# Kernel tuning notes

Measured on AMD Instinct MI355X. Metric: run time of the kernel, lower is better.

## Reference

```python
import jax, jax.numpy as jnp
import numpy as np

B, T, F, H = 2048, 512, 32, 128  # batch, seq_len, input_features, hidden_units

def _xavier(key, shape):
    fan_in, fan_out = shape[1], shape[0]
    limit = float(np.sqrt(6.0 / (fan_in + fan_out)))
    return jax.random.uniform(key, shape, jnp.float32, -limit, limit)

def setup_inputs() -> dict:
    key = jax.random.key(0)
    ks = jax.random.split(key, 8)
    x = jax.random.normal(ks[0], (B, T, F), jnp.float32)
    # PyTorch LSTM weights: weight_ih_l{k} [4H, in], weight_hh_l{k} [4H, H]; biases init to zeros.
    Wih0 = _xavier(ks[1], (4 * H, F))
    Whh0 = _xavier(ks[2], (4 * H, H))
    b0 = jnp.zeros((4 * H,), jnp.float32)  # b_ih + b_hh (both zero-init)
    Wih1 = _xavier(ks[3], (4 * H, H))
    Whh1 = _xavier(ks[4], (4 * H, H))
    b1 = jnp.zeros((4 * H,), jnp.float32)
    Wfc = _xavier(ks[5], (1, H))
    bfc = jnp.zeros((1,), jnp.float32)
    return dict(x=x, Wih0=Wih0, Whh0=Whh0, b0=b0, Wih1=Wih1, Whh1=Whh1, b1=b1, Wfc=Wfc, bfc=bfc)

def _lstm_layer(x, Wih, Whh, b):
    # x: [B, T, Din] -> outputs h over time: [B, T, H]
    pre = jnp.einsum('btf,gf->btg', x, Wih) + b  # precompute input projections [B, T, 4H]
    h0 = jnp.zeros((x.shape[0], Whh.shape[1]), x.dtype)

    def step(carry, p_t):
        h, c = carry
        z = p_t + h @ Whh.T  # [B, 4H]
        i, f, g, o = jnp.split(z, 4, axis=-1)  # PyTorch gate order: i, f, g, o
        i = jax.nn.sigmoid(i)
        f = jax.nn.sigmoid(f)
        g = jnp.tanh(g)
        o = jax.nn.sigmoid(o)
        c = f * c + i * g
        h = o * jnp.tanh(c)
        return (h, c), h

    (_, _), hs = jax.lax.scan(step, (h0, h0), jnp.swapaxes(pre, 0, 1))  # hs: [T, B, H]
    return jnp.swapaxes(hs, 0, 1)

def reference(x, Wih0, Whh0, b0, Wih1, Whh1, b1, Wfc, bfc):
    h = _lstm_layer(x, Wih0, Whh0, b0)   # layer 0 (dropout off in eval)
    h = _lstm_layer(h, Wih1, Whh1, b1)   # layer 1
    last = h[:, -1, :]                   # [B, H]
    return last @ Wfc.T + bfc            # [B, 1]
```

## Files before the change

### kernel.cpp

```cpp
#include <hip/hip_runtime.h>
#include <stdint.h>


#define B_ 2048
#define T_ 512
#define F_ 32
#define H_ 128
#define LSTR 144
#define H0SZ (8 * LSTR)
#define WIH1_NSTR 520
#define WIH1_WSTR (16 * WIH1_NSTR)

#define LOG2E 1.4426950408889634f

typedef _Float16 half8 __attribute__((ext_vector_type(8)));
typedef float float4_t __attribute__((ext_vector_type(4)));

#define BARRIER_LGKM() asm volatile("s_waitcnt lgkmcnt(0)\n\ts_barrier" ::: "memory")

__device__ __forceinline__ float fexp2(float x) {
  float r; asm("v_exp_f32 %0, %1" : "=v"(r) : "v"(x)); return r;
}
__device__ __forceinline__ float frcp(float x) { return __builtin_amdgcn_rcpf(x); }

__device__ __forceinline__ half8 cvt2f4(float4_t a, float4_t b) {
  half8 r;
  r[0] = (_Float16)a[0]; r[1] = (_Float16)a[1]; r[2] = (_Float16)a[2]; r[3] = (_Float16)a[3];
  r[4] = (_Float16)b[0]; r[5] = (_Float16)b[1]; r[6] = (_Float16)b[2]; r[7] = (_Float16)b[3];
  return r;
}
__device__ __forceinline__ half8 load8cvt(const float* p) {
  return cvt2f4(*(const float4_t*)p, *(const float4_t*)(p + 4));
}

__global__ __launch_bounds__(512, 2) void lstm_fused(
    const float* __restrict__ x, const float* __restrict__ Wih0,
    const float* __restrict__ Whh0, const float* __restrict__ b0,
    const float* __restrict__ Wih1, const float* __restrict__ Whh1,
    const float* __restrict__ b1, const float* __restrict__ Wfc,
    const float* __restrict__ bfc, float* __restrict__ out)
{
  __shared__ __attribute__((aligned(16))) _Float16 lds_wih1[8 * WIH1_WSTR];
  __shared__ __attribute__((aligned(16))) _Float16 lds_h0[2 * H0SZ];
  __shared__ __attribute__((aligned(16))) _Float16 lds_h1[2 * H0SZ];
  __shared__ float lds_fc[8][8];

  const int tid  = threadIdx.x;
  const int w    = tid >> 6;
  const int lane = tid & 63;
  const int n    = lane & 15;
  const int q    = lane >> 4;
  const int rbase = (int)blockIdx.x * 8;
  const int rload = rbase + (n & 7);
  const int rsh  = (q >> 1) * 2;
  const int rowq = (q & 1) * 4;
  const int colg = w * 16 + n;
  const int aoff = (n & 7) * LSTR + q * 8;

  half8 bwih0[4], bwhh0[4][4], bwhh1[4][4];
  _Float16* wslot = lds_wih1 + w * WIH1_WSTR + n * WIH1_NSTR + q * 8;
#pragma unroll
  for (int j = 0; j < 4; ++j) {
    const int g = j * H_ + colg;
    bwih0[j] = load8cvt(Wih0 + g * F_ + q * 8);
#pragma unroll
    for (int kc = 0; kc < 4; ++kc) {
      bwhh0[j][kc] = load8cvt(Whh0 + g * H_ + kc * 32 + q * 8);
      bwhh1[j][kc] = load8cvt(Whh1 + g * H_ + kc * 32 + q * 8);
      *(half8*)(wslot + (j * 4 + kc) * 32) = load8cvt(Wih1 + g * H_ + kc * 32 + q * 8);
    }
  }
  const float cI0 = -b0[0 * H_ + colg] * LOG2E;
  const float cF0 = -b0[1 * H_ + colg] * LOG2E;
  const float cG0 =  b0[2 * H_ + colg] * (2.0f * LOG2E);
  const float cO0 = -b0[3 * H_ + colg] * LOG2E;
  const float cI1 = -b1[0 * H_ + colg] * LOG2E;
  const float cF1 = -b1[1 * H_ + colg] * LOG2E;
  const float cG1 =  b1[2 * H_ + colg] * (2.0f * LOG2E);
  const float cO1 = -b1[3 * H_ + colg] * LOG2E;
  const float wfc = Wfc[colg];

  for (int i = tid; i < 2 * H0SZ; i += 512) { lds_h0[i] = (_Float16)0.0f; lds_h1[i] = (_Float16)0.0f; }
  __syncthreads();

  const float4_t zC = {0.f, 0.f, 0.f, 0.f};
  float c00 = 0.f, c01 = 0.f;
  float c10 = 0.f, c11 = 0.f;
  float hl0 = 0.f, hl1 = 0.f;

  const float* xptr = x + rload * (T_ * F_) + q * 8;
  float4_t xrA = *(const float4_t*)(xptr);
  float4_t xrB = *(const float4_t*)(xptr + 4);

#pragma unroll 1
  for (int tau = 0; tau <= T_; ++tau) {
    const int pw = tau & 1;
    _Float16* h0rd = lds_h0 + (pw ^ 1) * H0SZ;
    _Float16* h0wr = lds_h0 + pw * H0SZ;
    _Float16* h1rd = lds_h1 + pw * H0SZ;
    _Float16* h1wr = lds_h1 + (pw ^ 1) * H0SZ;
    const bool do0 = (tau < T_), do1 = (tau >= 1);

    half8 ah[4];
#pragma unroll
    for (int kc = 0; kc < 4; ++kc)
      ah[kc] = *(const half8*)(h0rd + aoff + kc * 32);

    float4_t acc0[4], acc1[4];
    if (do0) {
      half8 ax = cvt2f4(xrA, xrB);
#pragma unroll
      for (int j = 0; j < 4; ++j)
        acc0[j] = __builtin_amdgcn_mfma_f32_16x16x32_f16(ax, bwih0[j], zC, 0, 0, 0);
#pragma unroll
      for (int kc = 0; kc < 4; ++kc)
#pragma unroll
        for (int j = 0; j < 4; ++j)
          acc0[j] = __builtin_amdgcn_mfma_f32_16x16x32_f16(ah[kc], bwhh0[j][kc], acc0[j], 0, 0, 0);
      const int tn = (tau + 1 < T_) ? tau + 1 : T_ - 1;
      xrA = *(const float4_t*)(xptr + tn * F_);
      xrB = *(const float4_t*)(xptr + tn * F_ + 4);
    }
    if (do1) {
      half8 a1h[4];
#pragma unroll
      for (int kc = 0; kc < 4; ++kc)
        a1h[kc] = *(const half8*)(h1rd + aoff + kc * 32);
#pragma unroll
      for (int kc = 0; kc < 4; ++kc) {
        half8 f0 = *(const half8*)(wslot + (0 * 4 + kc) * 32);
        half8 f1 = *(const half8*)(wslot + (1 * 4 + kc) * 32);
        half8 f2 = *(const half8*)(wslot + (2 * 4 + kc) * 32);
        half8 f3 = *(const half8*)(wslot + (3 * 4 + kc) * 32);
        acc1[0] = __builtin_amdgcn_mfma_f32_16x16x32_f16(ah[kc], f0, kc == 0 ? zC : acc1[0], 0, 0, 0);
        acc1[1] = __builtin_amdgcn_mfma_f32_16x16x32_f16(ah[kc], f1, kc == 0 ? zC : acc1[1], 0, 0, 0);
        acc1[2] = __builtin_amdgcn_mfma_f32_16x16x32_f16(ah[kc], f2, kc == 0 ? zC : acc1[2], 0, 0, 0);
        acc1[3] = __builtin_amdgcn_mfma_f32_16x16x32_f16(ah[kc], f3, kc == 0 ? zC : acc1[3], 0, 0, 0);
      }
#pragma unroll
      for (int kc = 0; kc < 4; ++kc)
#pragma unroll
        for (int j = 0; j < 4; ++j)
          acc1[j] = __builtin_amdgcn_mfma_f32_16x16x32_f16(a1h[kc], bwhh1[j][kc], acc1[j], 0, 0, 0);
    }

    if (do0) {
#pragma unroll
      for (int rr = 0; rr < 2; ++rr) {
        const int ri = rsh + rr;
        const float gi = frcp(1.0f + fexp2(__builtin_fmaf(acc0[0][ri], -LOG2E, cI0)));
        const float gf = frcp(1.0f + fexp2(__builtin_fmaf(acc0[1][ri], -LOG2E, cF0)));
        const float gg = 1.0f - 2.0f * frcp(1.0f + fexp2(__builtin_fmaf(acc0[2][ri], 2.0f * LOG2E, cG0)));
        const float go = frcp(1.0f + fexp2(__builtin_fmaf(acc0[3][ri], -LOG2E, cO0)));
        float& cc = rr ? c01 : c00;
        cc = __builtin_fmaf(gf, cc, gi * gg);
        const float th = 1.0f - 2.0f * frcp(1.0f + fexp2(cc * (2.0f * LOG2E)));
        h0wr[(rowq + ri) * LSTR + colg] = (_Float16)(go * th);
      }
    }
    if (do1) {
#pragma unroll
      for (int rr = 0; rr < 2; ++rr) {
        const int ri = rsh + rr;
        const float gi = frcp(1.0f + fexp2(__builtin_fmaf(acc1[0][ri], -LOG2E, cI1)));
        const float gf = frcp(1.0f + fexp2(__builtin_fmaf(acc1[1][ri], -LOG2E, cF1)));
        const float gg = 1.0f - 2.0f * frcp(1.0f + fexp2(__builtin_fmaf(acc1[2][ri], 2.0f * LOG2E, cG1)));
        const float go = frcp(1.0f + fexp2(__builtin_fmaf(acc1[3][ri], -LOG2E, cO1)));
        float& cc = rr ? c11 : c10;
        cc = __builtin_fmaf(gf, cc, gi * gg);
        const float th = 1.0f - 2.0f * frcp(1.0f + fexp2(cc * (2.0f * LOG2E)));
        const float hv = go * th;
        h1wr[(rowq + ri) * LSTR + colg] = (_Float16)hv;
        if (rr) hl1 = hv; else hl0 = hv;
      }
    }
    BARRIER_LGKM();
  }

  float p0 = hl0 * wfc, p1 = hl1 * wfc;
#pragma unroll
  for (int m = 1; m < 16; m <<= 1) {
    p0 += __shfl_xor(p0, m);
    p1 += __shfl_xor(p1, m);
  }
  if (n == 0) {
    lds_fc[w][rowq + rsh + 0] = p0;
    lds_fc[w][rowq + rsh + 1] = p1;
  }
  __syncthreads();
  if (tid < 8) {
    float s = bfc[0];
#pragma unroll
    for (int wv = 0; wv < 8; ++wv) s += lds_fc[wv][tid];
    out[rbase + tid] = s;
  }
}

extern "C" void kernel_launch(void* const* d_in, const int* in_sizes, int n_in,
                              void* d_out, int out_size, void* d_ws, size_t ws_size,
                              hipStream_t stream) {
  const float* x    = (const float*)d_in[0];
  const float* Wih0 = (const float*)d_in[1];
  const float* Whh0 = (const float*)d_in[2];
  const float* b0   = (const float*)d_in[3];
  const float* Wih1 = (const float*)d_in[4];
  const float* Whh1 = (const float*)d_in[5];
  const float* b1   = (const float*)d_in[6];
  const float* Wfc  = (const float*)d_in[7];
  const float* bfc  = (const float*)d_in[8];
  float* outp = (float*)d_out;
  (void)d_ws; (void)ws_size;

  lstm_fused<<<B_ / 8, 512, 0, stream>>>(x, Wih0, Whh0, b0, Wih1, Whh1, b1,
                                         Wfc, bfc, outp);
}
```

Before: 1.054 ms.

## Hold half of Wih1 in registers, reorder layer-1 MFMAs, pack biases to fp16

Half of the layer-1 input weights (first two K-chunks) now stay in registers, and the remaining half moves to a smaller, contiguous LDS layout that is loaded in two staged groups interleaved with the MFMA chain. Layer-1 MFMAs move after the layer-0 gate math, so layer-0 h is written before layer-1 work. Biases are packed into one fp16 vector and the final h1 is read back from LDS, both to cut live registers. The goal is to reduce LDS traffic and latency per step while staying within the 2-blocks-per-CU register budget. The risks are spilling from extra register weights and lost precision in the fp16 biases and fp16 final h.

```diff
diff --git a/kernel.cpp b/kernel.cpp
--- a/kernel.cpp
+++ b/kernel.cpp
@@ -8,8 +8,7 @@
 #define H_ 128
 #define LSTR 144
 #define H0SZ (8 * LSTR)
-#define WIH1_NSTR 520
-#define WIH1_WSTR (16 * WIH1_NSTR)
+#define W1STR 4096
 
 #define LOG2E 1.4426950408889634f
 
@@ -40,7 +39,7 @@
     const float* __restrict__ b1, const float* __restrict__ Wfc,
     const float* __restrict__ bfc, float* __restrict__ out)
 {
-  __shared__ __attribute__((aligned(16))) _Float16 lds_wih1[8 * WIH1_WSTR];
+  __shared__ __attribute__((aligned(16))) _Float16 lds_w1[8 * W1STR];
   __shared__ __attribute__((aligned(16))) _Float16 lds_h0[2 * H0SZ];
   __shared__ __attribute__((aligned(16))) _Float16 lds_h1[2 * H0SZ];
   __shared__ float lds_fc[8][8];
@@ -57,8 +56,8 @@
   const int colg = w * 16 + n;
   const int aoff = (n & 7) * LSTR + q * 8;
 
-  half8 bwih0[4], bwhh0[4][4], bwhh1[4][4];
-  _Float16* wslot = lds_wih1 + w * WIH1_WSTR + n * WIH1_NSTR + q * 8;
+  half8 bwih0[4], bwhh0[4][4], bwhh1[4][4], bwih1r[2][4];
+  _Float16* w1base = lds_w1 + w * W1STR + q * 128 + n * 8;
 #pragma unroll
   for (int j = 0; j < 4; ++j) {
     const int g = j * H_ + colg;
@@ -67,18 +66,21 @@
     for (int kc = 0; kc < 4; ++kc) {
       bwhh0[j][kc] = load8cvt(Whh0 + g * H_ + kc * 32 + q * 8);
       bwhh1[j][kc] = load8cvt(Whh1 + g * H_ + kc * 32 + q * 8);
-      *(half8*)(wslot + (j * 4 + kc) * 32) = load8cvt(Wih1 + g * H_ + kc * 32 + q * 8);
-    }
-  }
-  const float cI0 = -b0[0 * H_ + colg] * LOG2E;
-  const float cF0 = -b0[1 * H_ + colg] * LOG2E;
-  const float cG0 =  b0[2 * H_ + colg] * (2.0f * LOG2E);
-  const float cO0 = -b0[3 * H_ + colg] * LOG2E;
-  const float cI1 = -b1[0 * H_ + colg] * LOG2E;
-  const float cF1 = -b1[1 * H_ + colg] * LOG2E;
-  const float cG1 =  b1[2 * H_ + colg] * (2.0f * LOG2E);
-  const float cO1 = -b1[3 * H_ + colg] * LOG2E;
-  const float wfc = Wfc[colg];
+    }
+    bwih1r[0][j] = load8cvt(Wih1 + g * H_ + 0 * 32 + q * 8);
+    bwih1r[1][j] = load8cvt(Wih1 + g * H_ + 1 * 32 + q * 8);
+    *(half8*)(w1base + (j * 2 + 0) * 512) = load8cvt(Wih1 + g * H_ + 2 * 32 + q * 8);
+    *(half8*)(w1base + (j * 2 + 1) * 512) = load8cvt(Wih1 + g * H_ + 3 * 32 + q * 8);
+  }
+  half8 cpack;
+  cpack[0] = (_Float16)(-b0[0 * H_ + colg] * LOG2E);
+  cpack[1] = (_Float16)(-b0[1 * H_ + colg] * LOG2E);
+  cpack[2] = (_Float16)( b0[2 * H_ + colg] * (2.0f * LOG2E));
+  cpack[3] = (_Float16)(-b0[3 * H_ + colg] * LOG2E);
+  cpack[4] = (_Float16)(-b1[0 * H_ + colg] * LOG2E);
+  cpack[5] = (_Float16)(-b1[1 * H_ + colg] * LOG2E);
+  cpack[6] = (_Float16)( b1[2 * H_ + colg] * (2.0f * LOG2E));
+  cpack[7] = (_Float16)(-b1[3 * H_ + colg] * LOG2E);
 
   for (int i = tid; i < 2 * H0SZ; i += 512) { lds_h0[i] = (_Float16)0.0f; lds_h1[i] = (_Float16)0.0f; }
   __syncthreads();
@@ -86,7 +88,6 @@
   const float4_t zC = {0.f, 0.f, 0.f, 0.f};
   float c00 = 0.f, c01 = 0.f;
   float c10 = 0.f, c11 = 0.f;
-  float hl0 = 0.f, hl1 = 0.f;
 
   const float* xptr = x + rload * (T_ * F_) + q * 8;
   float4_t xrA = *(const float4_t*)(xptr);
@@ -105,8 +106,12 @@
 #pragma unroll
     for (int kc = 0; kc < 4; ++kc)
       ah[kc] = *(const half8*)(h0rd + aoff + kc * 32);
-
-    float4_t acc0[4], acc1[4];
+    half8 w1s0[4];
+#pragma unroll
+    for (int j = 0; j < 4; ++j)
+      w1s0[j] = *(const half8*)(w1base + (j * 2 + 0) * 512);
+
+    float4_t acc0[4];
     if (do0) {
       half8 ax = cvt2f4(xrA, xrB);
 #pragma unroll
@@ -121,37 +126,14 @@
       xrA = *(const float4_t*)(xptr + tn * F_);
       xrB = *(const float4_t*)(xptr + tn * F_ + 4);
     }
-    if (do1) {
-      half8 a1h[4];
-#pragma unroll
-      for (int kc = 0; kc < 4; ++kc)
-        a1h[kc] = *(const half8*)(h1rd + aoff + kc * 32);
-#pragma unroll
-      for (int kc = 0; kc < 4; ++kc) {
-        half8 f0 = *(const half8*)(wslot + (0 * 4 + kc) * 32);
-        half8 f1 = *(const half8*)(wslot + (1 * 4 + kc) * 32);
-        half8 f2 = *(const half8*)(wslot + (2 * 4 + kc) * 32);
-        half8 f3 = *(const half8*)(wslot + (3 * 4 + kc) * 32);
-        acc1[0] = __builtin_amdgcn_mfma_f32_16x16x32_f16(ah[kc], f0, kc == 0 ? zC : acc1[0], 0, 0, 0);
-        acc1[1] = __builtin_amdgcn_mfma_f32_16x16x32_f16(ah[kc], f1, kc == 0 ? zC : acc1[1], 0, 0, 0);
-        acc1[2] = __builtin_amdgcn_mfma_f32_16x16x32_f16(ah[kc], f2, kc == 0 ? zC : acc1[2], 0, 0, 0);
-        acc1[3] = __builtin_amdgcn_mfma_f32_16x16x32_f16(ah[kc], f3, kc == 0 ? zC : acc1[3], 0, 0, 0);
-      }
-#pragma unroll
-      for (int kc = 0; kc < 4; ++kc)
-#pragma unroll
-        for (int j = 0; j < 4; ++j)
-          acc1[j] = __builtin_amdgcn_mfma_f32_16x16x32_f16(a1h[kc], bwhh1[j][kc], acc1[j], 0, 0, 0);
-    }
-
     if (do0) {
 #pragma unroll
       for (int rr = 0; rr < 2; ++rr) {
         const int ri = rsh + rr;
-        const float gi = frcp(1.0f + fexp2(__builtin_fmaf(acc0[0][ri], -LOG2E, cI0)));
-        const float gf = frcp(1.0f + fexp2(__builtin_fmaf(acc0[1][ri], -LOG2E, cF0)));
-        const float gg = 1.0f - 2.0f * frcp(1.0f + fexp2(__builtin_fmaf(acc0[2][ri], 2.0f * LOG2E, cG0)));
-        const float go = frcp(1.0f + fexp2(__builtin_fmaf(acc0[3][ri], -LOG2E, cO0)));
+        const float gi = frcp(1.0f + fexp2(__builtin_fmaf(acc0[0][ri], -LOG2E, (float)cpack[0])));
+        const float gf = frcp(1.0f + fexp2(__builtin_fmaf(acc0[1][ri], -LOG2E, (float)cpack[1])));
+        const float gg = 1.0f - 2.0f * frcp(1.0f + fexp2(__builtin_fmaf(acc0[2][ri], 2.0f * LOG2E, (float)cpack[2])));
+        const float go = frcp(1.0f + fexp2(__builtin_fmaf(acc0[3][ri], -LOG2E, (float)cpack[3])));
         float& cc = rr ? c01 : c00;
         cc = __builtin_fmaf(gf, cc, gi * gg);
         const float th = 1.0f - 2.0f * frcp(1.0f + fexp2(cc * (2.0f * LOG2E)));
@@ -159,25 +141,51 @@
       }
     }
     if (do1) {
+      float4_t acc1[4];
+#pragma unroll
+      for (int j = 0; j < 4; ++j)
+        acc1[j] = __builtin_amdgcn_mfma_f32_16x16x32_f16(ah[0], bwih1r[0][j], zC, 0, 0, 0);
+#pragma unroll
+      for (int j = 0; j < 4; ++j)
+        acc1[j] = __builtin_amdgcn_mfma_f32_16x16x32_f16(ah[1], bwih1r[1][j], acc1[j], 0, 0, 0);
+#pragma unroll
+      for (int j = 0; j < 4; ++j)
+        acc1[j] = __builtin_amdgcn_mfma_f32_16x16x32_f16(ah[2], w1s0[j], acc1[j], 0, 0, 0);
+      half8 w1s1[4];
+#pragma unroll
+      for (int j = 0; j < 4; ++j)
+        w1s1[j] = *(const half8*)(w1base + (j * 2 + 1) * 512);
+      half8 a1h[4];
+#pragma unroll
+      for (int kc = 0; kc < 4; ++kc)
+        a1h[kc] = *(const half8*)(h1rd + aoff + kc * 32);
+#pragma unroll
+      for (int j = 0; j < 4; ++j)
+        acc1[j] = __builtin_amdgcn_mfma_f32_16x16x32_f16(ah[3], w1s1[j], acc1[j], 0, 0, 0);
+#pragma unroll
+      for (int kc = 0; kc < 4; ++kc)
+#pragma unroll
+        for (int j = 0; j < 4; ++j)
+          acc1[j] = __builtin_amdgcn_mfma_f32_16x16x32_f16(a1h[kc], bwhh1[j][kc], acc1[j], 0, 0, 0);
 #pragma unroll
       for (int rr = 0; rr < 2; ++rr) {
         const int ri = rsh + rr;
-        const float gi = frcp(1.0f + fexp2(__builtin_fmaf(acc1[0][ri], -LOG2E, cI1)));
-        const float gf = frcp(1.0f + fexp2(__builtin_fmaf(acc1[1][ri], -LOG2E, cF1)));
-        const float gg = 1.0f - 2.0f * frcp(1.0f + fexp2(__builtin_fmaf(acc1[2][ri], 2.0f * LOG2E, cG1)));
-        const float go = frcp(1.0f + fexp2(__builtin_fmaf(acc1[3][ri], -LOG2E, cO1)));
+        const float gi = frcp(1.0f + fexp2(__builtin_fmaf(acc1[0][ri], -LOG2E, (float)cpack[4])));
+        const float gf = frcp(1.0f + fexp2(__builtin_fmaf(acc1[1][ri], -LOG2E, (float)cpack[5])));
+        const float gg = 1.0f - 2.0f * frcp(1.0f + fexp2(__builtin_fmaf(acc1[2][ri], 2.0f * LOG2E, (float)cpack[6])));
+        const float go = frcp(1.0f + fexp2(__builtin_fmaf(acc1[3][ri], -LOG2E, (float)cpack[7])));
         float& cc = rr ? c11 : c10;
         cc = __builtin_fmaf(gf, cc, gi * gg);
         const float th = 1.0f - 2.0f * frcp(1.0f + fexp2(cc * (2.0f * LOG2E)));
-        const float hv = go * th;
-        h1wr[(rowq + ri) * LSTR + colg] = (_Float16)hv;
-        if (rr) hl1 = hv; else hl0 = hv;
+        h1wr[(rowq + ri) * LSTR + colg] = (_Float16)(go * th);
       }
     }
     BARRIER_LGKM();
   }
 
-  float p0 = hl0 * wfc, p1 = hl1 * wfc;
+  const float wfcv = Wfc[colg];
+  float p0 = (float)lds_h1[H0SZ + (rowq + rsh + 0) * LSTR + colg] * wfcv;
+  float p1 = (float)lds_h1[H0SZ + (rowq + rsh + 1) * LSTR + colg] * wfcv;
 #pragma unroll
   for (int m = 1; m < 16; m <<= 1) {
     p0 += __shfl_xor(p0, m);
```

After: 1.234 ms. +17.0%, slower.

## Reorder layer-1 MFMA schedule with double-buffered Wih1 LDS fragments and conflict-free layout

Applied to the files above, without the earlier changes.

The LDS layout of the layer-1 input weights changes to a lane-contiguous stride (q*128 + n*8) that avoids bank conflicts. Loads of those fragments are spread across the loop, double-buffered between w1a and w1b, and the layer-1 MFMAs move after the layer-0 gate math so the LDS reads overlap with compute. The final FC reads h1 from LDS in fp16 instead of keeping fp32 copies in registers, which saves registers but adds a little rounding error.

```diff
diff --git a/kernel.cpp b/kernel.cpp
--- a/kernel.cpp
+++ b/kernel.cpp
@@ -8,8 +8,7 @@
 #define H_ 128
 #define LSTR 144
 #define H0SZ (8 * LSTR)
-#define WIH1_NSTR 520
-#define WIH1_WSTR (16 * WIH1_NSTR)
+#define W1STR 8192
 
 #define LOG2E 1.4426950408889634f
 
@@ -40,7 +39,7 @@
     const float* __restrict__ b1, const float* __restrict__ Wfc,
     const float* __restrict__ bfc, float* __restrict__ out)
 {
-  __shared__ __attribute__((aligned(16))) _Float16 lds_wih1[8 * WIH1_WSTR];
+  __shared__ __attribute__((aligned(16))) _Float16 lds_w1[8 * W1STR];
   __shared__ __attribute__((aligned(16))) _Float16 lds_h0[2 * H0SZ];
   __shared__ __attribute__((aligned(16))) _Float16 lds_h1[2 * H0SZ];
   __shared__ float lds_fc[8][8];
@@ -58,7 +57,7 @@
   const int aoff = (n & 7) * LSTR + q * 8;
 
   half8 bwih0[4], bwhh0[4][4], bwhh1[4][4];
-  _Float16* wslot = lds_wih1 + w * WIH1_WSTR + n * WIH1_NSTR + q * 8;
+  _Float16* w1base = lds_w1 + w * W1STR + q * 128 + n * 8;
 #pragma unroll
   for (int j = 0; j < 4; ++j) {
     const int g = j * H_ + colg;
@@ -67,7 +66,7 @@
     for (int kc = 0; kc < 4; ++kc) {
       bwhh0[j][kc] = load8cvt(Whh0 + g * H_ + kc * 32 + q * 8);
       bwhh1[j][kc] = load8cvt(Whh1 + g * H_ + kc * 32 + q * 8);
-      *(half8*)(wslot + (j * 4 + kc) * 32) = load8cvt(Wih1 + g * H_ + kc * 32 + q * 8);
+      *(half8*)(w1base + (kc * 4 + j) * 512) = load8cvt(Wih1 + g * H_ + kc * 32 + q * 8);
     }
   }
   const float cI0 = -b0[0 * H_ + colg] * LOG2E;
@@ -78,7 +77,6 @@
   const float cF1 = -b1[1 * H_ + colg] * LOG2E;
   const float cG1 =  b1[2 * H_ + colg] * (2.0f * LOG2E);
   const float cO1 = -b1[3 * H_ + colg] * LOG2E;
-  const float wfc = Wfc[colg];
 
   for (int i = tid; i < 2 * H0SZ; i += 512) { lds_h0[i] = (_Float16)0.0f; lds_h1[i] = (_Float16)0.0f; }
   __syncthreads();
@@ -86,7 +84,6 @@
   const float4_t zC = {0.f, 0.f, 0.f, 0.f};
   float c00 = 0.f, c01 = 0.f;
   float c10 = 0.f, c11 = 0.f;
-  float hl0 = 0.f, hl1 = 0.f;
 
   const float* xptr = x + rload * (T_ * F_) + q * 8;
   float4_t xrA = *(const float4_t*)(xptr);
@@ -105,8 +102,12 @@
 #pragma unroll
     for (int kc = 0; kc < 4; ++kc)
       ah[kc] = *(const half8*)(h0rd + aoff + kc * 32);
-
-    float4_t acc0[4], acc1[4];
+    half8 w1a[4];
+#pragma unroll
+    for (int j = 0; j < 4; ++j)
+      w1a[j] = *(const half8*)(w1base + (0 * 4 + j) * 512);
+
+    float4_t acc0[4];
     if (do0) {
       half8 ax = cvt2f4(xrA, xrB);
 #pragma unroll
@@ -121,29 +122,6 @@
       xrA = *(const float4_t*)(xptr + tn * F_);
       xrB = *(const float4_t*)(xptr + tn * F_ + 4);
     }
-    if (do1) {
-      half8 a1h[4];
-#pragma unroll
-      for (int kc = 0; kc < 4; ++kc)
-        a1h[kc] = *(const half8*)(h1rd + aoff + kc * 32);
-#pragma unroll
-      for (int kc = 0; kc < 4; ++kc) {
-        half8 f0 = *(const half8*)(wslot + (0 * 4 + kc) * 32);
-        half8 f1 = *(const half8*)(wslot + (1 * 4 + kc) * 32);
-        half8 f2 = *(const half8*)(wslot + (2 * 4 + kc) * 32);
-        half8 f3 = *(const half8*)(wslot + (3 * 4 + kc) * 32);
-        acc1[0] = __builtin_amdgcn_mfma_f32_16x16x32_f16(ah[kc], f0, kc == 0 ? zC : acc1[0], 0, 0, 0);
-        acc1[1] = __builtin_amdgcn_mfma_f32_16x16x32_f16(ah[kc], f1, kc == 0 ? zC : acc1[1], 0, 0, 0);
-        acc1[2] = __builtin_amdgcn_mfma_f32_16x16x32_f16(ah[kc], f2, kc == 0 ? zC : acc1[2], 0, 0, 0);
-        acc1[3] = __builtin_amdgcn_mfma_f32_16x16x32_f16(ah[kc], f3, kc == 0 ? zC : acc1[3], 0, 0, 0);
-      }
-#pragma unroll
-      for (int kc = 0; kc < 4; ++kc)
-#pragma unroll
-        for (int j = 0; j < 4; ++j)
-          acc1[j] = __builtin_amdgcn_mfma_f32_16x16x32_f16(a1h[kc], bwhh1[j][kc], acc1[j], 0, 0, 0);
-    }
-
     if (do0) {
 #pragma unroll
       for (int rr = 0; rr < 2; ++rr) {
@@ -159,6 +137,38 @@
       }
     }
     if (do1) {
+      float4_t acc1[4];
+      half8 w1b[4];
+#pragma unroll
+      for (int j = 0; j < 4; ++j)
+        w1b[j] = *(const half8*)(w1base + (1 * 4 + j) * 512);
+#pragma unroll
+      for (int j = 0; j < 4; ++j)
+        acc1[j] = __builtin_amdgcn_mfma_f32_16x16x32_f16(ah[0], w1a[j], zC, 0, 0, 0);
+#pragma unroll
+      for (int j = 0; j < 4; ++j)
+        w1a[j] = *(const half8*)(w1base + (2 * 4 + j) * 512);
+#pragma unroll
+      for (int j = 0; j < 4; ++j)
+        acc1[j] = __builtin_amdgcn_mfma_f32_16x16x32_f16(ah[1], w1b[j], acc1[j], 0, 0, 0);
+#pragma unroll
+      for (int j = 0; j < 4; ++j)
+        w1b[j] = *(const half8*)(w1base + (3 * 4 + j) * 512);
+#pragma unroll
+      for (int j = 0; j < 4; ++j)
+        acc1[j] = __builtin_amdgcn_mfma_f32_16x16x32_f16(ah[2], w1a[j], acc1[j], 0, 0, 0);
+      half8 a1h[4];
+#pragma unroll
+      for (int kc = 0; kc < 4; ++kc)
+        a1h[kc] = *(const half8*)(h1rd + aoff + kc * 32);
+#pragma unroll
+      for (int j = 0; j < 4; ++j)
+        acc1[j] = __builtin_amdgcn_mfma_f32_16x16x32_f16(ah[3], w1b[j], acc1[j], 0, 0, 0);
+#pragma unroll
+      for (int kc = 0; kc < 4; ++kc)
+#pragma unroll
+        for (int j = 0; j < 4; ++j)
+          acc1[j] = __builtin_amdgcn_mfma_f32_16x16x32_f16(a1h[kc], bwhh1[j][kc], acc1[j], 0, 0, 0);
 #pragma unroll
       for (int rr = 0; rr < 2; ++rr) {
         const int ri = rsh + rr;
@@ -169,15 +179,15 @@
         float& cc = rr ? c11 : c10;
         cc = __builtin_fmaf(gf, cc, gi * gg);
         const float th = 1.0f - 2.0f * frcp(1.0f + fexp2(cc * (2.0f * LOG2E)));
-        const float hv = go * th;
-        h1wr[(rowq + ri) * LSTR + colg] = (_Float16)hv;
-        if (rr) hl1 = hv; else hl0 = hv;
+        h1wr[(rowq + ri) * LSTR + colg] = (_Float16)(go * th);
       }
     }
     BARRIER_LGKM();
   }
 
-  float p0 = hl0 * wfc, p1 = hl1 * wfc;
+  const float wfcv = Wfc[colg];
+  float p0 = (float)lds_h1[H0SZ + (rowq + rsh + 0) * LSTR + colg] * wfcv;
+  float p1 = (float)lds_h1[H0SZ + (rowq + rsh + 1) * LSTR + colg] * wfcv;
 #pragma unroll
   for (int m = 1; m < 16; m <<= 1) {
     p0 += __shfl_xor(p0, m);
```

New measurement: 980.4 us. 7.0% less time.
